# Kernel optimization log

Measured on AMD Instinct MI355X. Metric: run time of the kernel, lower is better.

Reference implementation:

```python
import jax, jax.numpy as jnp
import numpy as np

EPS = 1e-5

def conv2d(x, w, b=None, stride=1, pad=0):
    # x: NCHW, w: OIHW
    y = jax.lax.conv_general_dilated(x, w, (stride, stride), [(pad, pad), (pad, pad)],
                                     dimension_numbers=('NCHW', 'OIHW', 'NCHW'))
    if b is not None:
        y = y + b[None, :, None, None]
    return y

def bn_eval(x, g, b, m, v):
    inv = jax.lax.rsqrt(v + EPS)
    return (x - m[None, :, None, None]) * (g * inv)[None, :, None, None] + b[None, :, None, None]

def setup_inputs() -> dict:
    key = jax.random.key(0)
    ks = jax.random.split(key, 20)
    B, Cin, Cout, H, W = 2, 64, 64, 96, 96
    Cqk = Cout // 4
    d = {}
    d['x'] = jax.random.normal(ks[0], (B, Cin, H, W), jnp.float32)
    # pre_conv: 3x3 conv (no bias) + BN + ReLU
    d['w_pre'] = jax.random.normal(ks[1], (Cout, Cin, 3, 3), jnp.float32) * 0.05
    d['bn1_g'] = jax.random.normal(ks[2], (Cout,), jnp.float32) * 0.1 + 1.0
    d['bn1_b'] = jax.random.normal(ks[3], (Cout,), jnp.float32) * 0.1
    d['bn1_m'] = jax.random.normal(ks[4], (Cout,), jnp.float32) * 0.1
    d['bn1_v'] = jax.random.uniform(ks[5], (Cout,), jnp.float32) + 0.5
    # 1x1 q/k/v convs (with bias, as nn.Conv2d default)
    d['wq'] = jax.random.normal(ks[6], (Cqk, Cout, 1, 1), jnp.float32) * 0.05
    d['bq'] = jax.random.normal(ks[7], (Cqk,), jnp.float32) * 0.01
    d['wk'] = jax.random.normal(ks[8], (Cqk, Cout, 1, 1), jnp.float32) * 0.05
    d['bk'] = jax.random.normal(ks[9], (Cqk,), jnp.float32) * 0.01
    d['wv'] = jax.random.normal(ks[10], (Cout, Cout, 1, 1), jnp.float32) * 0.05
    d['bv'] = jax.random.normal(ks[11], (Cout,), jnp.float32) * 0.01
    # final_conv: 3x3 conv (no bias) + BN + ReLU
    d['w_fin'] = jax.random.normal(ks[12], (Cout, Cout, 3, 3), jnp.float32) * 0.05
    d['bn2_g'] = jax.random.normal(ks[13], (Cout,), jnp.float32) * 0.1 + 1.0
    d['bn2_b'] = jax.random.normal(ks[14], (Cout,), jnp.float32) * 0.1
    d['bn2_m'] = jax.random.normal(ks[15], (Cout,), jnp.float32) * 0.1
    d['bn2_v'] = jax.random.uniform(ks[16], (Cout,), jnp.float32) + 0.5
    d['gamma'] = jnp.array([0.5], jnp.float32)  # nonzero so attention path contributes
    return d

def reference(x, w_pre, bn1_g, bn1_b, bn1_m, bn1_v, wq, bq, wk, bk, wv, bv,
              w_fin, bn2_g, bn2_b, bn2_m, bn2_v, gamma):
    # pre_conv: Conv3x3 + BN(eval) + ReLU
    x = jax.nn.relu(bn_eval(conv2d(x, w_pre, None, 1, 1), bn1_g, bn1_b, bn1_m, bn1_v))
    B, C, H, W = x.shape
    N = H * W
    q = conv2d(x, wq, bq).reshape(B, -1, N)   # (B, C/4, N)
    k = conv2d(x, wk, bk).reshape(B, -1, N)   # (B, C/4, N)
    v = conv2d(x, wv, bv).reshape(B, C, N)    # (B, C, N)
    energy = jnp.einsum('bci,bcj->bij', q, k)         # (B, N, N)
    attn = jax.nn.softmax(energy, axis=-1)
    # out[b,c,i] = sum_j v[b,c,j] * attn[b,i,j]  (bmm(V, attn^T) in torch)
    out = jnp.einsum('bcj,bij->bci', v, attn).reshape(B, C, H, W)
    out_feat = gamma[0] * out + x
    out_feat = jax.nn.relu(bn_eval(conv2d(out_feat, w_fin, None, 1, 1), bn2_g, bn2_b, bn2_m, bn2_v))
    return out_feat
```

## Files before the change

kernel.cpp:

```cpp
#include <hip/hip_runtime.h>
#include <hip/hip_bf16.h>


using short8 = __attribute__((ext_vector_type(8))) short;
using f32x4  = __attribute__((ext_vector_type(4))) float;
using f32x16 = __attribute__((ext_vector_type(16))) float;
using u32x4  = __attribute__((ext_vector_type(4))) unsigned;
typedef unsigned u32;
typedef unsigned short ushort;

#define NPIX 9216
#define PW 98
#define PLANE 9604
#define PLANEB 9608
#define SEG 240
#define LOG2E 1.44269504088896340736f

__device__ __forceinline__ ushort f2bf(float f) {
  u32 x = __builtin_bit_cast(u32, f);
  return (ushort)((x + 0x7fffu + ((x >> 16) & 1u)) >> 16);
}
__device__ __forceinline__ float bf2f(ushort h) {
  return __builtin_bit_cast(float, (u32)h << 16);
}

__global__ __launch_bounds__(256) void wprep(
    const float* __restrict__ w_pre, const float* __restrict__ w_fin,
    ushort* __restrict__ fpre, ushort* __restrict__ ffin)
{
  const int i = blockIdx.x * 256 + threadIdx.x;
  const float* w = blockIdx.y ? w_fin : w_pre;
  ushort* dst    = blockIdx.y ? ffin : fpre;
  const int kk = i & 7, l = (i >> 3) & 63, cot = (i >> 9) & 1;
  const int chunk = (i >> 10) & 3, tap = i >> 12;
  const int co = cot * 32 + (l & 31);
  const int ci = chunk * 16 + 8 * (l >> 5) + kk;
  const float wv = w[co * 576 + ci * 9 + tap];
  const ushort h = f2bf(wv);
  const ushort lo = f2bf(wv - bf2f(h));
  const int base = tap * 8192 + chunk * 2048 + cot * 1024 + l * 8 + kk;
  dst[base] = h;
  dst[base + 512] = lo;
}

__global__ __launch_bounds__(256) void pad_split(
    const float* __restrict__ in, ushort* __restrict__ xh, ushort* __restrict__ xl)
{
  const int plane = blockIdx.x;
  const float* src = in + (size_t)plane * 9216;
  const size_t dbase = (size_t)plane * PLANEB;
  for (int idx = threadIdx.x; idx < 9216; idx += 256) {
    const int y = idx / 96, x = idx - y * 96;
    const float v = src[idx];
    const ushort h = f2bf(v);
    const size_t d = dbase + (y + 1) * PW + x + 1;
    xh[d] = h;
    xl[d] = f2bf(v - bf2f(h));
  }
}

template <bool PADOUT>
__global__ __launch_bounds__(128) void conv3x3_mfma(
    const ushort* __restrict__ xh, const ushort* __restrict__ xl,
    const ushort* __restrict__ wfrag,
    const float* __restrict__ gg, const float* __restrict__ bb_,
    const float* __restrict__ mm, const float* __restrict__ vv,
    float* __restrict__ outp)
{
  __shared__ ushort stage[2][SEG][18];
  __shared__ float scb[64], shb[64];
  const int n0  = blockIdx.x * 32;
  const int b   = blockIdx.y;
  const int tid = threadIdx.x;
  const int wm  = tid >> 6;
  const int lane = tid & 63;
  const int li = lane & 31, hi = lane >> 5;

  if (tid < 64) {
    const float sc = gg[tid] * rsqrtf(vv[tid] + 1e-5f);
    scb[tid] = sc;
    shb[tid] = bb_[tid] - mm[tid] * sc;
  }

  f32x16 acc = {};
  const int sbase = n0 - 8;

  for (int chunk = 0; chunk < 4; ++chunk) {
    __syncthreads();
#pragma unroll
    for (int it = 0; it < 8; ++it) {
      const int item = tid + it * 128;
      if (item < 960) {
        const int pl   = item >= 480;
        const int rem  = pl ? item - 480 : item;
        const int eblk = rem >> 4;
        const int ci   = rem & 15;
        const ushort* src = (pl ? xl : xh) +
            (size_t)(b * 64 + chunk * 16 + ci) * PLANEB + sbase + eblk * 8;
        const short8 v = *(const short8*)src;
#pragma unroll
        for (int j = 0; j < 8; ++j) stage[pl][eblk * 8 + j][ci] = (ushort)v[j];
      }
    }
    __syncthreads();

    const ushort* wb0 = wfrag + (size_t)(chunk * 2048 + wm * 1024 + lane * 8);
    short8 ah = *(const short8*)(wb0);
    short8 al = *(const short8*)(wb0 + 512);
#pragma unroll
    for (int tap = 0; tap < 9; ++tap) {
      const int eoff = (tap / 3) * PW + (tap % 3) + 7 + li;
      const short8 bh = *(const short8*)&stage[0][eoff][hi * 8];
      const short8 bl = *(const short8*)&stage[1][eoff][hi * 8];
      short8 ahn, aln;
      if (tap < 8) {
        const ushort* wbn = wb0 + (size_t)(tap + 1) * 8192;
        ahn = *(const short8*)(wbn);
        aln = *(const short8*)(wbn + 512);
      }
      acc = __builtin_amdgcn_mfma_f32_32x32x16_bf16(ah, bh, acc, 0, 0, 0);
      acc = __builtin_amdgcn_mfma_f32_32x32x16_bf16(ah, bl, acc, 0, 0, 0);
      acc = __builtin_amdgcn_mfma_f32_32x32x16_bf16(al, bh, acc, 0, 0, 0);
      acc = __builtin_amdgcn_mfma_f32_32x32x16_bf16(al, bl, acc, 0, 0, 0);
      if (tap < 8) { ah = ahn; al = aln; }
    }
  }

  const int pix = n0 + li;
  const int y = pix / PW;
  const int x = pix - y * PW;
  if (x >= 1 && x <= 96) {
#pragma unroll
    for (int r = 0; r < 16; ++r) {
      const int co = wm * 32 + (r & 3) + 8 * (r >> 2) + 4 * hi;
      const float val = fmaxf(scb[co] * acc[r] + shb[co], 0.f);
      if (PADOUT)
        outp[(size_t)(b * 64 + co) * PLANE + pix + PW] = val;
      else
        outp[(size_t)(b * 64 + co) * 9216 + y * 96 + (x - 1)] = val;
    }
  }
}

__global__ __launch_bounds__(64) void qkv_kernel(
    const float* __restrict__ x1p,
    const float* __restrict__ wq, const float* __restrict__ bq,
    const float* __restrict__ wk, const float* __restrict__ bk,
    const float* __restrict__ wv, const float* __restrict__ bv,
    ushort* __restrict__ qsp, ushort* __restrict__ ksp,
    ushort* __restrict__ vfrag)
{
  const int pix0 = blockIdx.x * 16;
  const int cot  = blockIdx.y;
  const int b    = blockIdx.z;
  const int lane = threadIdx.x;
  const int g    = lane >> 4;
  const int col  = lane & 15;

  const float* wr;
  const float* bias;
  if (cot == 0)      { wr = wq + col * 64; bias = bq; }
  else if (cot == 1) { wr = wk + col * 64; bias = bk; }
  else               { wr = wv + ((cot - 2) * 16 + col) * 64; bias = bv + (cot - 2) * 16; }

  const int yy = pix0 / 96, xx = pix0 - yy * 96;
  const int ro = (yy + 1) * PW + xx + 1;

  f32x4 acc = (f32x4){0.f, 0.f, 0.f, 0.f};
  const float* xb = x1p + (size_t)b * 64 * PLANE;
#pragma unroll
  for (int kt = 0; kt < 2; ++kt) {
    const float4 wa = *(const float4*)(wr + kt * 32 + 8 * g);
    const float4 wb2 = *(const float4*)(wr + kt * 32 + 8 * g + 4);
    short8 af;
    af[0] = (short)f2bf(wa.x); af[1] = (short)f2bf(wa.y);
    af[2] = (short)f2bf(wa.z); af[3] = (short)f2bf(wa.w);
    af[4] = (short)f2bf(wb2.x); af[5] = (short)f2bf(wb2.y);
    af[6] = (short)f2bf(wb2.z); af[7] = (short)f2bf(wb2.w);
    short8 bf;
#pragma unroll
    for (int jj = 0; jj < 8; ++jj)
      bf[jj] = (short)f2bf(xb[(size_t)(kt * 32 + 8 * g + jj) * PLANE + ro + col]);
    acc = __builtin_amdgcn_mfma_f32_16x16x32_bf16(af, bf, acc, 0, 0, 0);
  }
  if (cot < 2) {
    ushort* dst = (cot == 0 ? qsp : ksp) + ((size_t)(b * NPIX + pix0 + col)) * 32;
    const float scl = (cot == 0) ? LOG2E : 1.f;
#pragma unroll
    for (int r = 0; r < 4; ++r) {
      const int cl = 4 * g + r;
      const float val = (acc[r] + bias[cl]) * scl;
      const ushort h = f2bf(val);
      dst[cl] = h;
      dst[16 + cl] = f2bf(val - bf2f(h));
    }
  } else {
    ushort* dst = vfrag + (size_t)b * 589824;
    const int pix = pix0 + col;
    const int jt = pix >> 5, ks = (pix >> 4) & 1;
    const int lhalf = 32 * ((pix >> 3) & 1);
    const int kk = pix & 7;
#pragma unroll
    for (int r = 0; r < 4; ++r) {
      const int cl = 4 * g + r;
      const int c = (cot - 2) * 16 + cl;
      const int h = c >> 5;
      const int lA = (c & 31) + lhalf;
      dst[(size_t)((((jt * 2 + h) * 2 + ks) * 64 + lA)) * 8 + kk] =
          f2bf(acc[r] + bias[cl]);
    }
  }
}

__global__ __launch_bounds__(256, 3) void attn_kernel(
    const ushort* __restrict__ qsp, const ushort* __restrict__ ksp,
    const ushort* __restrict__ vfrag, const float* __restrict__ x1p,
    const float* __restrict__ gamma_p,
    ushort* __restrict__ ofh, ushort* __restrict__ ofl)
{
  __shared__ float2 mlb[4][64];
  __shared__ float obuf[64][65];
  __shared__ float lbuf[64];

  const int b   = blockIdx.y;
  const int i0  = blockIdx.x * 64;
  const int tid = threadIdx.x;
  const int w   = tid >> 6;
  const int lane = tid & 63;
  const int li  = lane & 31;
  const int hi  = lane >> 5;

  for (int idx = tid; idx < 64 * 65; idx += 256) ((float*)obuf)[idx] = 0.f;
  if (tid < 64) lbuf[tid] = 0.f;
  __syncthreads();

  const ushort* kb    = ksp + (size_t)b * NPIX * 32;
  const ushort* vbase = vfrag + (size_t)b * 589824;

  short8 qfh[2], qfl[2];
#pragma unroll
  for (int qh = 0; qh < 2; ++qh) {
    const ushort* qrow = qsp + ((size_t)b * NPIX + i0 + qh * 32 + li) * 32 + 8 * hi;
    qfh[qh] = *(const short8*)(qrow);
    qfl[qh] = *(const short8*)(qrow + 16);
  }

  float m[2] = {-INFINITY, -INFINITY};
  float lsum[2] = {0.f, 0.f};
  f32x16 acc[2][2] = {};

  const int jt0 = w * 72;
  const ushort* kptr = kb + (size_t)(jt0 * 32 + li) * 32 + 8 * hi;
  const ushort* vptr = vbase + ((size_t)(jt0 * 4) * 64 + lane) * 8;

  short8 kfh  = *(const short8*)kptr;
  short8 kfl  = *(const short8*)(kptr + 16);
  short8 vf00 = *(const short8*)(vptr);
  short8 vf01 = *(const short8*)(vptr + 512);
  short8 vf10 = *(const short8*)(vptr + 1024);
  short8 vf11 = *(const short8*)(vptr + 1536);

  const f32x16 zf = {};
  for (int t = 0; t < 72; ++t) {
    f32x16 sv[2];
#pragma unroll
    for (int qh = 0; qh < 2; ++qh) {
      sv[qh] = __builtin_amdgcn_mfma_f32_32x32x16_bf16(kfh, qfh[qh], zf, 0, 0, 0);
      sv[qh] = __builtin_amdgcn_mfma_f32_32x32x16_bf16(kfl, qfh[qh], sv[qh], 0, 0, 0);
      sv[qh] = __builtin_amdgcn_mfma_f32_32x32x16_bf16(kfh, qfl[qh], sv[qh], 0, 0, 0);
    }

    short8 kfh_n, kfl_n, v00n, v01n, v10n, v11n;
    if (t < 71) {
      kptr += 1024; vptr += 2048;
      kfh_n = *(const short8*)kptr;
      kfl_n = *(const short8*)(kptr + 16);
      v00n = *(const short8*)(vptr);
      v01n = *(const short8*)(vptr + 512);
      v10n = *(const short8*)(vptr + 1024);
      v11n = *(const short8*)(vptr + 1536);
    }

#pragma unroll
    for (int qh = 0; qh < 2; ++qh) {
      f32x16 s = sv[qh];
      float pm = fmaxf(fmaxf(fmaxf(s[0], s[1]), fmaxf(s[2], s[3])),
                       fmaxf(fmaxf(s[4], s[5]), fmaxf(s[6], s[7])));
      pm = fmaxf(pm, fmaxf(fmaxf(fmaxf(s[8], s[9]), fmaxf(s[10], s[11])),
                           fmaxf(fmaxf(s[12], s[13]), fmaxf(s[14], s[15]))));
      {
        float o = pm;
        asm("v_permlane32_swap_b32 %0, %1" : "+v"(o), "+v"(pm));
        pm = fmaxf(pm, o);
      }

      if (__any(pm > m[qh] + 8.f)) {
        const float mnew = fmaxf(m[qh], pm);
        const float corr = __builtin_amdgcn_exp2f(m[qh] - mnew);
        lsum[qh] *= corr;
        acc[qh][0] *= corr;
        acc[qh][1] *= corr;
        m[qh] = mnew;
      }

#pragma unroll
      for (int r = 0; r < 16; ++r) s[r] = __builtin_amdgcn_exp2f(s[r] - m[qh]);
      float ps = (((s[0] + s[1]) + (s[2] + s[3])) + ((s[4] + s[5]) + (s[6] + s[7]))) +
                 (((s[8] + s[9]) + (s[10] + s[11])) + ((s[12] + s[13]) + (s[14] + s[15])));
      {
        float o = ps;
        asm("v_permlane32_swap_b32 %0, %1" : "+v"(o), "+v"(ps));
        ps = ps + o;
      }
      lsum[qh] += ps;

      u32 c01, c23, c45, c67, d01, d23, d45, d67;
      asm("v_cvt_pk_bf16_f32 %0, %1, %2" : "=v"(c01) : "v"(s[0]),  "v"(s[1]));
      asm("v_cvt_pk_bf16_f32 %0, %1, %2" : "=v"(c23) : "v"(s[2]),  "v"(s[3]));
      asm("v_cvt_pk_bf16_f32 %0, %1, %2" : "=v"(c45) : "v"(s[4]),  "v"(s[5]));
      asm("v_cvt_pk_bf16_f32 %0, %1, %2" : "=v"(c67) : "v"(s[6]),  "v"(s[7]));
      asm("v_cvt_pk_bf16_f32 %0, %1, %2" : "=v"(d01) : "v"(s[8]),  "v"(s[9]));
      asm("v_cvt_pk_bf16_f32 %0, %1, %2" : "=v"(d23) : "v"(s[10]), "v"(s[11]));
      asm("v_cvt_pk_bf16_f32 %0, %1, %2" : "=v"(d45) : "v"(s[12]), "v"(s[13]));
      asm("v_cvt_pk_bf16_f32 %0, %1, %2" : "=v"(d67) : "v"(s[14]), "v"(s[15]));
      asm("v_permlane32_swap_b32 %0, %1" : "+v"(c45), "+v"(c01));
      asm("v_permlane32_swap_b32 %0, %1" : "+v"(c67), "+v"(c23));
      asm("v_permlane32_swap_b32 %0, %1" : "+v"(d45), "+v"(d01));
      asm("v_permlane32_swap_b32 %0, %1" : "+v"(d67), "+v"(d23));
      const short8 pf1 = __builtin_bit_cast(short8, (u32x4){c01, c23, c45, c67});
      const short8 pf2 = __builtin_bit_cast(short8, (u32x4){d01, d23, d45, d67});

      acc[qh][0] = __builtin_amdgcn_mfma_f32_32x32x16_bf16(vf00, pf1, acc[qh][0], 0, 0, 0);
      acc[qh][0] = __builtin_amdgcn_mfma_f32_32x32x16_bf16(vf01, pf2, acc[qh][0], 0, 0, 0);
      acc[qh][1] = __builtin_amdgcn_mfma_f32_32x32x16_bf16(vf10, pf1, acc[qh][1], 0, 0, 0);
      acc[qh][1] = __builtin_amdgcn_mfma_f32_32x32x16_bf16(vf11, pf2, acc[qh][1], 0, 0, 0);
    }

    if (t < 71) {
      kfh = kfh_n; kfl = kfl_n;
      vf00 = v00n; vf01 = v01n; vf10 = v10n; vf11 = v11n;
    }
  }

  if (hi == 0) {
#pragma unroll
    for (int qh = 0; qh < 2; ++qh) {
      float2 t2; t2.x = m[qh]; t2.y = lsum[qh];
      mlb[w][qh * 32 + li] = t2;
    }
  }
  __syncthreads();
  float f[2];
#pragma unroll
  for (int qh = 0; qh < 2; ++qh) {
    float M = -INFINITY;
#pragma unroll
    for (int ww = 0; ww < 4; ++ww) M = fmaxf(M, mlb[ww][qh * 32 + li].x);
    f[qh] = __builtin_amdgcn_exp2f(m[qh] - M);
  }
  if (hi == 0) {
#pragma unroll
    for (int qh = 0; qh < 2; ++qh) atomicAdd(&lbuf[qh * 32 + li], lsum[qh] * f[qh]);
  }
#pragma unroll
  for (int qh = 0; qh < 2; ++qh)
#pragma unroll
    for (int hh = 0; hh < 2; ++hh)
#pragma unroll
      for (int r = 0; r < 16; ++r) {
        const int c = (r & 3) + 8 * (r >> 2) + 4 * hi + 32 * hh;
        atomicAdd(&obuf[qh * 32 + li][c], acc[qh][hh][r] * f[qh]);
      }
  __syncthreads();

  const float gm = gamma_p[0];
  for (int idx = tid; idx < 4096; idx += 256) {
    const int il = idx & 63, c = idx >> 6;
    const int p = i0 + il;
    const int y = p / 96, x = p - y * 96;
    const int ro = (y + 1) * PW + x + 1;
    const float val = obuf[il][c] / lbuf[il] * gm +
                      x1p[(size_t)(b * 64 + c) * PLANE + ro];
    const ushort h = f2bf(val);
    const size_t d = (size_t)(b * 64 + c) * PLANEB + ro;
    ofh[d] = h;
    ofl[d] = f2bf(val - bf2f(h));
  }
}

extern "C" void kernel_launch(void* const* d_in, const int* in_sizes, int n_in,
                              void* d_out, int out_size, void* d_ws, size_t ws_size,
                              hipStream_t stream) {
  const float* x      = (const float*)d_in[0];
  const float* w_pre  = (const float*)d_in[1];
  const float* bn1_g  = (const float*)d_in[2];
  const float* bn1_b  = (const float*)d_in[3];
  const float* bn1_m  = (const float*)d_in[4];
  const float* bn1_v  = (const float*)d_in[5];
  const float* wq     = (const float*)d_in[6];
  const float* bq     = (const float*)d_in[7];
  const float* wk     = (const float*)d_in[8];
  const float* bk     = (const float*)d_in[9];
  const float* wv     = (const float*)d_in[10];
  const float* bv     = (const float*)d_in[11];
  const float* w_fin  = (const float*)d_in[12];
  const float* bn2_g  = (const float*)d_in[13];
  const float* bn2_b  = (const float*)d_in[14];
  const float* bn2_m  = (const float*)d_in[15];
  const float* bn2_v  = (const float*)d_in[16];
  const float* gamma  = (const float*)d_in[17];
  float* out = (float*)d_out;

  char* ws = (char*)d_ws;
  float*  x1p  = (float*)(ws);
  ushort* xh   = (ushort*)(ws + 4917248);
  ushort* xl   = (ushort*)(ws + 7376896);
  ushort* qsp  = (ushort*)(ws + 9836544);
  ushort* ksp  = (ushort*)(ws + 11016192);
  ushort* vfr  = (ushort*)(ws + 12195840);
  ushort* fpre = (ushort*)(ws + 14555136);
  ushort* ffin = (ushort*)(ws + 14702592);
  ushort* ofh = xh;
  ushort* ofl = xl;

  hipMemsetAsync(ws + 4917248, 0, 4919296, stream);

  wprep<<<dim3(144, 2), 256, 0, stream>>>(w_pre, w_fin, fpre, ffin);
  pad_split<<<dim3(128), 256, 0, stream>>>(x, xh, xl);
  conv3x3_mfma<true><<<dim3(294, 2), 128, 0, stream>>>(
      xh, xl, fpre, bn1_g, bn1_b, bn1_m, bn1_v, x1p);
  qkv_kernel<<<dim3(576, 6, 2), 64, 0, stream>>>(
      x1p, wq, bq, wk, bk, wv, bv, qsp, ksp, vfr);
  attn_kernel<<<dim3(144, 2), 256, 0, stream>>>(
      qsp, ksp, vfr, x1p, gamma, ofh, ofl);
  conv3x3_mfma<false><<<dim3(294, 2), 128, 0, stream>>>(
      ofh, ofl, ffin, bn2_g, bn2_b, bn2_m, bn2_v, out);
}
```

Measured before the change: 182.1 us.

## Split attention over key segments with a separate merge kernel

The attention kernel now splits the key dimension into 4 segments across the grid, giving 1152 blocks instead of 288. Each block writes a normalized partial output in bf16 plus its per-row max and sum. A new merge kernel combines the partials with log-sum-exp weights and applies the gamma residual. This is meant to fill the GPU's compute units better, at the cost of extra global traffic, an extra launch, and bf16 rounding of the partial outputs.

```diff
diff --git a/kernel.cpp b/kernel.cpp
--- a/kernel.cpp
+++ b/kernel.cpp
@@ -14,6 +14,7 @@
 #define PLANE 9604
 #define PLANEB 9608
 #define SEG 240
+#define NSEG 4
 #define LOG2E 1.44269504088896340736f
 
 __device__ __forceinline__ ushort f2bf(float f) {
@@ -214,16 +215,17 @@
 
 __global__ __launch_bounds__(256, 3) void attn_kernel(
     const ushort* __restrict__ qsp, const ushort* __restrict__ ksp,
-    const ushort* __restrict__ vfrag, const float* __restrict__ x1p,
-    const float* __restrict__ gamma_p,
-    ushort* __restrict__ ofh, ushort* __restrict__ ofl)
+    const ushort* __restrict__ vfrag,
+    ushort* __restrict__ pnum, float2* __restrict__ pml)
 {
   __shared__ float2 mlb[4][64];
   __shared__ float obuf[64][65];
   __shared__ float lbuf[64];
 
-  const int b   = blockIdx.y;
-  const int i0  = blockIdx.x * 64;
+  const int qb  = blockIdx.x;
+  const int seg = blockIdx.y;
+  const int b   = blockIdx.z;
+  const int i0  = qb * 64;
   const int tid = threadIdx.x;
   const int w   = tid >> 6;
   const int lane = tid & 63;
@@ -249,7 +251,7 @@
   float lsum[2] = {0.f, 0.f};
   f32x16 acc[2][2] = {};
 
-  const int jt0 = w * 72;
+  const int jt0 = seg * 72 + w * 18;
   const ushort* kptr = kb + (size_t)(jt0 * 32 + li) * 32 + 8 * hi;
   const ushort* vptr = vbase + ((size_t)(jt0 * 4) * 64 + lane) * 8;
 
@@ -261,7 +263,7 @@
   short8 vf11 = *(const short8*)(vptr + 1536);
 
   const f32x16 zf = {};
-  for (int t = 0; t < 72; ++t) {
+  for (int t = 0; t < 18; ++t) {
     f32x16 sv[2];
 #pragma unroll
     for (int qh = 0; qh < 2; ++qh) {
@@ -271,7 +273,7 @@
     }
 
     short8 kfh_n, kfl_n, v00n, v01n, v10n, v11n;
-    if (t < 71) {
+    if (t < 17) {
       kptr += 1024; vptr += 2048;
       kfh_n = *(const short8*)kptr;
       kfl_n = *(const short8*)(kptr + 16);
@@ -336,7 +338,7 @@
       acc[qh][1] = __builtin_amdgcn_mfma_f32_32x32x16_bf16(vf11, pf2, acc[qh][1], 0, 0, 0);
     }
 
-    if (t < 71) {
+    if (t < 17) {
       kfh = kfh_n; kfl = kfl_n;
       vf00 = v00n; vf01 = v01n; vf10 = v10n; vf11 = v11n;
     }
@@ -373,14 +375,54 @@
       }
   __syncthreads();
 
-  const float gm = gamma_p[0];
+  const size_t base = ((size_t)(b * 144 + qb)) * NSEG + seg;
+  ushort* pn = pnum + base * 4096;
   for (int idx = tid; idx < 4096; idx += 256) {
-    const int il = idx & 63, c = idx >> 6;
-    const int p = i0 + il;
-    const int y = p / 96, x = p - y * 96;
-    const int ro = (y + 1) * PW + x + 1;
-    const float val = obuf[il][c] / lbuf[il] * gm +
-                      x1p[(size_t)(b * 64 + c) * PLANE + ro];
+    const int i = idx & 63, c = idx >> 6;
+    pn[c * 64 + i] = f2bf(obuf[i][c] / lbuf[i]);
+  }
+  if (tid < 64) {
+    float M = fmaxf(fmaxf(mlb[0][tid].x, mlb[1][tid].x),
+                    fmaxf(mlb[2][tid].x, mlb[3][tid].x));
+    float2 t2; t2.x = M; t2.y = lbuf[tid];
+    pml[base * 64 + tid] = t2;
+  }
+}
+
+__global__ __launch_bounds__(256) void attn_merge(
+    const ushort* __restrict__ pnum, const float2* __restrict__ pml,
+    const float* __restrict__ x1p, const float* __restrict__ gamma_p,
+    ushort* __restrict__ ofh, ushort* __restrict__ ofl)
+{
+  const int qb = blockIdx.x;
+  const int b  = blockIdx.y;
+  const int tid = threadIdx.x;
+  const int il = tid & 63;
+  const int c0 = tid >> 6;
+  const size_t base0 = ((size_t)(b * 144 + qb)) * NSEG;
+
+  float2 ml[NSEG];
+#pragma unroll
+  for (int s = 0; s < NSEG; ++s) ml[s] = pml[(base0 + s) * 64 + il];
+  float M = fmaxf(fmaxf(ml[0].x, ml[1].x), fmaxf(ml[2].x, ml[3].x));
+  float wgt[NSEG], W = 0.f;
+#pragma unroll
+  for (int s = 0; s < NSEG; ++s) {
+    wgt[s] = ml[s].y * __builtin_amdgcn_exp2f(ml[s].x - M);
+    W += wgt[s];
+  }
+  const float scl = gamma_p[0] / W;
+
+  const int p = qb * 64 + il;
+  const int y = p / 96, x = p - y * 96;
+  const int ro = (y + 1) * PW + x + 1;
+
+  for (int c = c0; c < 64; c += 4) {
+    float sum = 0.f;
+#pragma unroll
+    for (int s = 0; s < NSEG; ++s)
+      sum += bf2f(pnum[(base0 + s) * 4096 + c * 64 + il]) * wgt[s];
+    const float val = sum * scl + x1p[(size_t)(b * 64 + c) * PLANE + ro];
     const ushort h = f2bf(val);
     const size_t d = (size_t)(b * 64 + c) * PLANEB + ro;
     ofh[d] = h;
@@ -420,6 +462,8 @@
   ushort* vfr  = (ushort*)(ws + 12195840);
   ushort* fpre = (ushort*)(ws + 14555136);
   ushort* ffin = (ushort*)(ws + 14702592);
+  ushort* pnum = (ushort*)(ws + 14850048);
+  float2* pml  = (float2*)(ws + 24287232);
   ushort* ofh = xh;
   ushort* ofl = xl;
 
@@ -431,8 +475,10 @@
       xh, xl, fpre, bn1_g, bn1_b, bn1_m, bn1_v, x1p);
   qkv_kernel<<<dim3(576, 6, 2), 64, 0, stream>>>(
       x1p, wq, bq, wk, bk, wv, bv, qsp, ksp, vfr);
-  attn_kernel<<<dim3(144, 2), 256, 0, stream>>>(
-      qsp, ksp, vfr, x1p, gamma, ofh, ofl);
+  attn_kernel<<<dim3(144, NSEG, 2), 256, 0, stream>>>(
+      qsp, ksp, vfr, pnum, pml);
+  attn_merge<<<dim3(144, 2), 256, 0, stream>>>(
+      pnum, pml, x1p, gamma, ofh, ofl);
   conv3x3_mfma<false><<<dim3(294, 2), 128, 0, stream>>>(
       ofh, ofl, ffin, bn2_g, bn2_b, bn2_m, bn2_v, out);
 }
```

Measured after the change: 220.7 us. 1.21x slower.
